# Kernel optimization log

Hardware: AMD Instinct MI355X
Metric: run time of the kernel (lower is better)

Reference implementation:

```python
import jax, jax.numpy as jnp
import numpy as np

NHEAD = 16
EPS = 1e-5

def layer_norm(x, g, b):
    mu = jnp.mean(x, axis=-1, keepdims=True)
    var = jnp.mean(jnp.square(x - mu), axis=-1, keepdims=True)
    return (x - mu) * jax.lax.rsqrt(var + EPS) * g + b

def setup_inputs() -> dict:
    key = jax.random.key(0)
    ks = jax.random.split(key, 12)
    d_model, d_hid = 1024, 4096  # MHA num_hiddens == dim_feedforward (source quirk)
    B, S = 2, 2048
    s_in = 1.0 / np.sqrt(d_model)
    s_hid = 1.0 / np.sqrt(d_hid)
    return {
        "x": jax.random.normal(ks[0], (B, S, d_model), jnp.float32),
        "Wq": jax.random.normal(ks[1], (d_model, d_hid), jnp.float32) * s_in,
        "Wk": jax.random.normal(ks[2], (d_model, d_hid), jnp.float32) * s_in,
        "Wv": jax.random.normal(ks[3], (d_model, d_hid), jnp.float32) * s_in,
        "Wo": jax.random.normal(ks[4], (d_hid, d_model), jnp.float32) * s_hid,
        "W1": jax.random.normal(ks[5], (d_model, d_hid), jnp.float32) * s_in,
        "b1": jnp.zeros((d_hid,), jnp.float32),
        "W2": jax.random.normal(ks[6], (d_hid, d_model), jnp.float32) * s_hid,
        "b2": jnp.zeros((d_model,), jnp.float32),
        "g1": jnp.ones((d_model,), jnp.float32),
        "be1": jnp.zeros((d_model,), jnp.float32),
        "g2": jnp.ones((d_model,), jnp.float32),
        "be2": jnp.zeros((d_model,), jnp.float32),
    }

def reference(x, Wq, Wk, Wv, Wo, W1, b1, W2, b2, g1, be1, g2, be2):
    B, S, D = x.shape
    H = NHEAD
    # pre-norm attention branch (dropout = identity at eval)
    x1 = layer_norm(x, g1, be1)
    q = (x1 @ Wq).reshape(B, S, H, -1)  # [B,S,H,dh], dh = num_hiddens/H
    k = (x1 @ Wk).reshape(B, S, H, -1)
    v = (x1 @ Wv).reshape(B, S, H, -1)
    dh = q.shape[-1]
    scores = jnp.einsum('bqhd,bkhd->bhqk', q, k) / jnp.sqrt(jnp.float32(dh))
    attn = jax.nn.softmax(scores, axis=-1)
    ctx = jnp.einsum('bhqk,bkhd->bqhd', attn, v).reshape(B, S, -1)
    x = x + ctx @ Wo
    # pre-norm FFN branch
    x2 = layer_norm(x, g2, be2)
    h = jax.nn.relu(x2 @ W1 + b1)
    out = x + (h @ W2 + b2)
    return out
```

## Files before the change

### kernel.cpp

```cpp
#include <hip/hip_runtime.h>
#include <hip/hip_bf16.h>
#include <stdint.h>

using bf16x8 = __attribute__((ext_vector_type(8))) __bf16;
using f32x4  = __attribute__((ext_vector_type(4))) float;

__device__ __forceinline__ uint16_t f2bf(float f) {
    uint32_t u = __builtin_bit_cast(uint32_t, f);
    u += 0x7FFFu + ((u >> 16) & 1u);
    return (uint16_t)(u >> 16);
}
__device__ __forceinline__ uint32_t pack2bf(float lo, float hi) {
    return (uint32_t)f2bf(lo) | ((uint32_t)f2bf(hi) << 16);
}

__device__ __forceinline__ void gld_lds16(const void* g, void* l) {
    __builtin_amdgcn_global_load_lds(
        (const __attribute__((address_space(1))) void*)g,
        (__attribute__((address_space(3))) void*)l,
        16, 0, 0);
}

__global__ __launch_bounds__(256)
void wconv(const float* __restrict__ in, uint16_t* __restrict__ out, int R, int C) {
    __shared__ float t[32][33];
    int c0 = blockIdx.x * 32, r0 = blockIdx.y * 32;
    int tx = threadIdx.x & 31, ty = threadIdx.x >> 5;
    #pragma unroll
    for (int i = 0; i < 32; i += 8)
        t[ty + i][tx] = in[(size_t)(r0 + ty + i) * C + c0 + tx];
    __syncthreads();
    #pragma unroll
    for (int i = 0; i < 32; i += 8)
        out[(size_t)(c0 + ty + i) * R + r0 + tx] = f2bf(t[tx][ty + i]);
}

__global__ __launch_bounds__(256)
void ln_bf16(const float* __restrict__ x, const float* __restrict__ gw,
             const float* __restrict__ bw, uint16_t* __restrict__ out) {
    const int D = 1024;
    int row = blockIdx.x;
    float4 v = ((const float4*)(x + (size_t)row * D))[threadIdx.x];
    float s  = v.x + v.y + v.z + v.w;
    float ss = v.x * v.x + v.y * v.y + v.z * v.z + v.w * v.w;
    #pragma unroll
    for (int m = 1; m < 64; m <<= 1) {
        s  += __shfl_xor(s, m);
        ss += __shfl_xor(ss, m);
    }
    __shared__ float red[8];
    int wid = threadIdx.x >> 6, lane = threadIdx.x & 63;
    if (lane == 0) { red[wid] = s; red[4 + wid] = ss; }
    __syncthreads();
    s  = red[0] + red[1] + red[2] + red[3];
    ss = red[4] + red[5] + red[6] + red[7];
    float mu  = s * (1.f / 1024.f);
    float var = ss * (1.f / 1024.f) - mu * mu;
    float rstd = rsqrtf(var + 1e-5f);
    float4 gv = ((const float4*)gw)[threadIdx.x];
    float4 bv = ((const float4*)bw)[threadIdx.x];
    ushort4 o;
    o.x = f2bf((v.x - mu) * rstd * gv.x + bv.x);
    o.y = f2bf((v.y - mu) * rstd * gv.y + bv.y);
    o.z = f2bf((v.z - mu) * rstd * gv.z + bv.z);
    o.w = f2bf((v.w - mu) * rstd * gv.w + bv.w);
    ((ushort4*)(out + (size_t)row * D))[threadIdx.x] = o;
}

template <int EPI>
__global__ __launch_bounds__(256, 2)
void gemm_bt(const uint16_t* __restrict__ A, const uint16_t* __restrict__ B,
             void* __restrict__ Cp, const float* __restrict__ bias,
             const float* __restrict__ resid, int M, int N, int K) {
    __shared__ uint16_t sA[128 * 32];
    __shared__ uint16_t sB[128 * 32];
    int bid = blockIdx.x;
    int cpx = gridDim.x >> 3;
    bid = (bid & 7) * cpx + (bid >> 3);
    int nbn  = N >> 7;
    int brow = (bid / nbn) << 7;
    int bcol = (bid % nbn) << 7;
    int t = threadIdx.x;
    int wid = t >> 6, lane = t & 63;
    int wr = (wid >> 1) << 6, wc = (wid & 1) << 6;
    int q = lane & 15, g = lane >> 4;

    f32x4 acc[4][4] = {};

    const uint16_t* Abase = A + (size_t)brow * K + ((lane & 3) << 3);
    const uint16_t* Bbase = B + (size_t)bcol * K + ((lane & 3) << 3);
    int rsub = lane >> 2;

    for (int kt = 0; kt < K; kt += 32) {
        __syncthreads();
        #pragma unroll
        for (int i = 0; i < 2; ++i) {
            int chunk = i * 4 + wid;
            int row = chunk * 16 + rsub;
            gld_lds16(Abase + (size_t)row * K + kt, &sA[chunk * 512]);
            gld_lds16(Bbase + (size_t)row * K + kt, &sB[chunk * 512]);
        }
        __syncthreads();
        bf16x8 af[4], bfr[4];
        #pragma unroll
        for (int i = 0; i < 4; ++i)
            af[i] = *(const bf16x8*)&sA[(wr + i * 16 + q) * 32 + g * 8];
        #pragma unroll
        for (int j = 0; j < 4; ++j)
            bfr[j] = *(const bf16x8*)&sB[(wc + j * 16 + q) * 32 + g * 8];
        #pragma unroll
        for (int i = 0; i < 4; ++i)
            #pragma unroll
            for (int j = 0; j < 4; ++j)
                acc[i][j] = __builtin_amdgcn_mfma_f32_16x16x32_bf16(
                    af[i], bfr[j], acc[i][j], 0, 0, 0);
    }

    float* Cf = (float*)Cp;
    #pragma unroll
    for (int i = 0; i < 4; ++i) {
        #pragma unroll
        for (int j = 0; j < 4; ++j) {
            #pragma unroll
            for (int r = 0; r < 4; ++r) {
                int gr = brow + wr + i * 16 + g * 4 + r;
                int gc = bcol + wc + j * 16 + q;
                float v = acc[i][j][r];
                size_t idx = (size_t)gr * N + gc;
                if constexpr (EPI == 2) {
                    Cf[idx] = v + bias[gc] + resid[idx];
                } else {
                    Cf[idx] = v + resid[idx];
                }
            }
        }
    }
}

template <int EPI>
__global__ __launch_bounds__(512, 2)
void gemm256(const uint16_t* __restrict__ A, const uint16_t* __restrict__ B,
             void* __restrict__ Cp, const float* __restrict__ bias,
             int M, int N, int K) {
    __shared__ uint8_t smem[131072];
    int bid = blockIdx.x;
    int cpx = gridDim.x >> 3;
    bid = (bid & 7) * cpx + (bid >> 3);
    int nbn  = N >> 8;
    int brow = (bid / nbn) << 8;
    int bcol = (bid % nbn) << 8;
    int t0 = threadIdx.x;
    int wid = t0 >> 6, lane = t0 & 63;
    int wr = wid >> 2, wc = wid & 3;
    int q = lane & 15, g = lane >> 4;

    const uint16_t* Asw = A + (size_t)(brow + (lane >> 3)) * K + (((lane & 7) ^ (lane >> 3)) << 3);
    const uint16_t* Bsw = B + (size_t)(bcol + (lane >> 3)) * K + (((lane & 7) ^ (lane >> 3)) << 3);

    f32x4 acc[2][2][4][2] = {};
    int NKT = K >> 6;

#define STAGE256(BSEL, KK)                                                     \
    {                                                                          \
        uint8_t* dA = smem + (BSEL) * 32768;                                   \
        uint8_t* dB = smem + 65536 + (BSEL) * 32768;                           \
        _Pragma("unroll")                                                      \
        for (int i = 0; i < 4; ++i) {                                          \
            int c = wid * 4 + i;                                               \
            gld_lds16(Asw + (size_t)(c * 8) * K + (KK), dA + c * 1024);        \
            gld_lds16(Bsw + (size_t)(c * 8) * K + (KK), dB + c * 1024);        \
        }                                                                      \
    }

    STAGE256(0, 0)

    for (int t = 0; t < NKT; ++t) {
        int cur = t & 1;
        if (t + 1 < NKT) {
            STAGE256(cur ^ 1, (t + 1) << 6)
            asm volatile("s_waitcnt vmcnt(8)" ::: "memory");
        } else {
            asm volatile("s_waitcnt vmcnt(0)" ::: "memory");
        }
        __builtin_amdgcn_sched_barrier(0);
        __builtin_amdgcn_s_barrier();
        __builtin_amdgcn_sched_barrier(0);

        const uint8_t* bA = smem + cur * 32768;
        const uint8_t* bB = smem + 65536 + cur * 32768;

        bf16x8 af[4][2], bfr[2][2];

#define LOADA256(MH)                                                           \
        _Pragma("unroll")                                                      \
        for (int m2 = 0; m2 < 4; ++m2)                                         \
            _Pragma("unroll")                                                  \
            for (int ks = 0; ks < 2; ++ks) {                                   \
                int rr = wr * 128 + (MH) * 64 + m2 * 16 + q;                   \
                int sl = (ks * 4 + g) ^ (q & 7);                               \
                af[m2][ks] = *(const bf16x8*)(bA + rr * 128 + sl * 16);        \
            }
#define LOADB256(NH)                                                           \
        _Pragma("unroll")                                                      \
        for (int n2 = 0; n2 < 2; ++n2)                                         \
            _Pragma("unroll")                                                  \
            for (int ks = 0; ks < 2; ++ks) {                                   \
                int cc = wc * 64 + (NH) * 32 + n2 * 16 + q;                    \
                int sl = (ks * 4 + g) ^ (q & 7);                               \
                bfr[n2][ks] = *(const bf16x8*)(bB + cc * 128 + sl * 16);       \
            }
#define MMQ256(MH, NH)                                                         \
        __builtin_amdgcn_s_setprio(1);                                         \
        _Pragma("unroll")                                                      \
        for (int m2 = 0; m2 < 4; ++m2)                                         \
            _Pragma("unroll")                                                  \
            for (int n2 = 0; n2 < 2; ++n2)                                     \
                _Pragma("unroll")                                              \
                for (int ks = 0; ks < 2; ++ks)                                 \
                    acc[MH][NH][m2][n2] = __builtin_amdgcn_mfma_f32_16x16x32_bf16( \
                        af[m2][ks], bfr[n2][ks], acc[MH][NH][m2][n2], 0, 0, 0);\
        __builtin_amdgcn_s_setprio(0);

        LOADA256(0) LOADB256(0) MMQ256(0, 0)
        LOADB256(1) MMQ256(0, 1)
        LOADA256(1) MMQ256(1, 1)
        LOADB256(0) MMQ256(1, 0)

        __builtin_amdgcn_s_barrier();
    }

    uint16_t* Cb = (uint16_t*)Cp;
    #pragma unroll
    for (int mh = 0; mh < 2; ++mh)
        #pragma unroll
        for (int nh = 0; nh < 2; ++nh)
            #pragma unroll
            for (int m2 = 0; m2 < 4; ++m2)
                #pragma unroll
                for (int n2 = 0; n2 < 2; ++n2)
                    #pragma unroll
                    for (int r = 0; r < 4; ++r) {
                        int gr = brow + wr * 128 + mh * 64 + m2 * 16 + g * 4 + r;
                        int gc = bcol + wc * 64 + nh * 32 + n2 * 16 + q;
                        float v = acc[mh][nh][m2][n2][r];
                        if constexpr (EPI == 1) {
                            v += bias[gc];
                            v = v > 0.f ? v : 0.f;
                        }
                        Cb[(size_t)gr * N + gc] = f2bf(v);
                    }
#undef STAGE256
#undef LOADA256
#undef LOADB256
#undef MMQ256
}

__device__ __forceinline__ void attn_stage(uint8_t* smem, int bufsel,
        const uint16_t* Kb0, const uint16_t* Vb0, int ktok, int wid, int lane) {
    #pragma unroll
    for (int i = 0; i < 4; ++i) {
        int chunk = wid * 4 + i;
        int r = 2 * chunk + (lane >> 5);
        int s = lane & 31;
        int cg = (s & ~7) | ((s ^ r) & 7);
        gld_lds16(Kb0 + (size_t)(ktok + r) * 8192 + cg * 8,
                  smem + bufsel * 16384 + chunk * 1024);
    }
    #pragma unroll
    for (int i = 0; i < 4; ++i) {
        int chunk = wid * 4 + i;
        int r = 16 * chunk + (lane >> 2);
        int s = lane & 3;
        int cg = s ^ (r & 3);
        gld_lds16(Vb0 + (size_t)r * 4096 + ktok + cg * 8,
                  smem + 32768 + bufsel * 16384 + chunk * 1024);
    }
}

__device__ __forceinline__ bf16x8 sm_pack(const f32x4* sacc, f32x4* acc,
                                          float& m_run, float& l_run,
                                          int q, int g) {
    float mx = fmaxf(fmaxf(fmaxf(sacc[0][0], sacc[0][1]), fmaxf(sacc[0][2], sacc[0][3])),
                     fmaxf(fmaxf(sacc[1][0], sacc[1][1]), fmaxf(sacc[1][2], sacc[1][3])));
    mx = fmaxf(mx, __shfl_xor(mx, 16));
    mx = fmaxf(mx, __shfl_xor(mx, 32));
    if (!__all(mx - m_run <= 8.f)) {
        float m_new = fmaxf(m_run, mx);
        float alpha = __expf(m_run - m_new);
        l_run *= alpha;
        #pragma unroll
        for (int td = 0; td < 16; ++td) {
            acc[td][0] *= alpha; acc[td][1] *= alpha;
            acc[td][2] *= alpha; acc[td][3] *= alpha;
        }
        m_run = m_new;
    }
    float p[8]; float rs = 0.f;
    #pragma unroll
    for (int tm = 0; tm < 2; ++tm)
        #pragma unroll
        for (int r = 0; r < 4; ++r) {
            float e = __expf(sacc[tm][r] - m_run);
            p[tm * 4 + r] = e; rs += e;
        }
    rs += __shfl_xor(rs, 16);
    rs += __shfl_xor(rs, 32);
    l_run += rs;

    uint32_t pk0 = pack2bf(p[0], p[1]);
    uint32_t pk1 = pack2bf(p[2], p[3]);
    uint32_t pk2 = pack2bf(p[4], p[5]);
    uint32_t pk3 = pack2bf(p[6], p[7]);
    int srcA = ((g & 1) << 5) + q;
    int srcB = srcA + 16;
    uint32_t a0 = __shfl(pk0, srcA), a1 = __shfl(pk2, srcA);
    uint32_t b0 = __shfl(pk1, srcA), b1 = __shfl(pk3, srcA);
    uint32_t c0 = __shfl(pk0, srcB), c1 = __shfl(pk2, srcB);
    uint32_t d0 = __shfl(pk1, srcB), d1 = __shfl(pk3, srcB);
    bool hi = g >= 2;
    uint4 pb;
    pb.x = hi ? a1 : a0;
    pb.y = hi ? b1 : b0;
    pb.z = hi ? c1 : c0;
    pb.w = hi ? d1 : d0;
    return __builtin_bit_cast(bf16x8, pb);
}

__global__ __launch_bounds__(256, 2)
void attn(const uint16_t* __restrict__ Qg, const uint16_t* __restrict__ Kg,
          const uint16_t* __restrict__ Vtg, uint16_t* __restrict__ Og) {
    const int S = 2048, NT = 64, QKS = 8192, OC = 4096;
    __shared__ uint8_t smem[65536];

    int id = blockIdx.x;
    id = (id & 7) * 64 + (id >> 3);
    int qb = id & 15, h = (id >> 4) & 15, b = id >> 8;

    int t = threadIdx.x;
    int wid = t >> 6, lane = t & 63;
    int q = lane & 15, g = lane >> 4;
    int tok0 = b * S + qb * 128 + wid * 32;

    bf16x8 qf0[8], qf1[8];
    {
        const uint16_t* qrow0 = Qg + (size_t)(tok0 + q) * QKS + h * 256 + g * 8;
        const uint16_t* qrow1 = Qg + (size_t)(tok0 + 16 + q) * QKS + h * 256 + g * 8;
        #pragma unroll
        for (int c = 0; c < 8; ++c) {
            bf16x8 r0 = *(const bf16x8*)(qrow0 + c * 32);
            bf16x8 r1 = *(const bf16x8*)(qrow1 + c * 32);
            #pragma unroll
            for (int i = 0; i < 8; ++i) {
                r0[i] = (__bf16)((float)r0[i] * 0.0625f);
                r1[i] = (__bf16)((float)r1[i] * 0.0625f);
            }
            qf0[c] = r0; qf1[c] = r1;
        }
    }

    f32x4 acc0[16] = {}, acc1[16] = {};
    float m0 = -1e30f, l0 = 0.f;
    float m1 = -1e30f, l1 = 0.f;

    const uint16_t* Kb0 = Kg + (size_t)(b * S) * QKS + h * 256;
    const uint16_t* Vb0 = Vtg + (size_t)(h * 256) * 4096 + b * S;

    attn_stage(smem, 0, Kb0, Vb0, 0, wid, lane);

    for (int kt = 0; kt < NT; ++kt) {
        int cb = (kt & 1) * 16384;
        if (kt + 1 < NT) {
            attn_stage(smem, (kt + 1) & 1, Kb0, Vb0, (kt + 1) * 32, wid, lane);
            asm volatile("s_waitcnt vmcnt(12)" ::: "memory");
        } else {
            asm volatile("s_waitcnt vmcnt(4)" ::: "memory");
        }
        __builtin_amdgcn_sched_barrier(0);
        __builtin_amdgcn_s_barrier();

        const uint16_t* sk = (const uint16_t*)(smem + cb);
        const uint16_t* sv = (const uint16_t*)(smem + 32768 + cb);

        f32x4 sA0[2] = {}, sA1[2] = {};
        __builtin_amdgcn_s_setprio(1);
        #pragma unroll
        for (int c = 0; c < 8; ++c) {
            #pragma unroll
            for (int tm = 0; tm < 2; ++tm) {
                int G = c * 4 + g;
                int slot = (G & ~7) | ((G ^ q) & 7);
                bf16x8 kf = *(const bf16x8*)(sk + (tm * 16 + q) * 256 + slot * 8);
                sA0[tm] = __builtin_amdgcn_mfma_f32_16x16x32_bf16(kf, qf0[c], sA0[tm], 0, 0, 0);
                sA1[tm] = __builtin_amdgcn_mfma_f32_16x16x32_bf16(kf, qf1[c], sA1[tm], 0, 0, 0);
            }
        }
        __builtin_amdgcn_s_setprio(0);

        bf16x8 pfrag0 = sm_pack(sA0, acc0, m0, l0, q, g);
        bf16x8 pfrag1 = sm_pack(sA1, acc1, m1, l1, q, g);

        if (kt + 1 < NT) {
            asm volatile("s_waitcnt vmcnt(8)" ::: "memory");
        } else {
            asm volatile("s_waitcnt vmcnt(0)" ::: "memory");
        }
        __builtin_amdgcn_sched_barrier(0);
        __builtin_amdgcn_s_barrier();

        int sl = g ^ (q & 3);
        __builtin_amdgcn_s_setprio(1);
        #pragma unroll
        for (int td = 0; td < 16; ++td) {
            bf16x8 vf = *(const bf16x8*)(sv + (td * 16 + q) * 32 + sl * 8);
            acc0[td] = __builtin_amdgcn_mfma_f32_16x16x32_bf16(vf, pfrag0, acc0[td], 0, 0, 0);
            acc1[td] = __builtin_amdgcn_mfma_f32_16x16x32_bf16(vf, pfrag1, acc1[td], 0, 0, 0);
        }
        __builtin_amdgcn_s_setprio(0);
        __builtin_amdgcn_s_barrier();
    }

    __syncthreads();
    {
        float inv0 = 1.f / l0, inv1 = 1.f / l1;
        uint32_t* w0 = (uint32_t*)(smem + wid * 16384);
        uint32_t* w1 = (uint32_t*)(smem + wid * 16384 + 8192);
        #pragma unroll
        for (int td = 0; td < 16; ++td) {
            int base = (q * 256 + td * 16 + g * 4) >> 1;
            w0[base]     = pack2bf(acc0[td][0] * inv0, acc0[td][1] * inv0);
            w0[base + 1] = pack2bf(acc0[td][2] * inv0, acc0[td][3] * inv0);
            w1[base]     = pack2bf(acc1[td][0] * inv1, acc1[td][1] * inv1);
            w1[base + 1] = pack2bf(acc1[td][2] * inv1, acc1[td][3] * inv1);
        }
    }
    __syncthreads();
    #pragma unroll
    for (int s2 = 0; s2 < 2; ++s2) {
        const uint16_t* tb = (const uint16_t*)(smem + wid * 16384 + s2 * 8192);
        #pragma unroll
        for (int r2 = 0; r2 < 8; ++r2) {
            int c = r2 * 64 + lane;
            int qq = c >> 5, dc = c & 31;
            uint4 v = *(const uint4*)&tb[qq * 256 + dc * 8];
            *(uint4*)(Og + (size_t)(tok0 + s2 * 16 + qq) * OC + h * 256 + dc * 8) = v;
        }
    }
}

extern "C" void kernel_launch(void* const* d_in, const int* in_sizes, int n_in,
                              void* d_out, int out_size, void* d_ws, size_t ws_size,
                              hipStream_t stream) {
    const float* x   = (const float*)d_in[0];
    const float* Wq  = (const float*)d_in[1];
    const float* Wk  = (const float*)d_in[2];
    const float* Wv  = (const float*)d_in[3];
    const float* Wo  = (const float*)d_in[4];
    const float* W1  = (const float*)d_in[5];
    const float* b1  = (const float*)d_in[6];
    const float* W2  = (const float*)d_in[7];
    const float* b2  = (const float*)d_in[8];
    const float* g1  = (const float*)d_in[9];
    const float* be1 = (const float*)d_in[10];
    const float* g2  = (const float*)d_in[11];
    const float* be2 = (const float*)d_in[12];

    char* ws = (char*)d_ws;
    const size_t M8 = 8388608;
    uint16_t* WqkT = (uint16_t*)(ws + 0 * M8);
    uint16_t* WqT  = WqkT;
    uint16_t* WkT  = (uint16_t*)(ws + 1 * M8);
    uint16_t* WvT  = (uint16_t*)(ws + 2 * M8);
    uint16_t* WoT  = (uint16_t*)(ws + 3 * M8);
    uint16_t* W1T  = (uint16_t*)(ws + 4 * M8);
    uint16_t* W2T  = (uint16_t*)(ws + 5 * M8);
    uint16_t* x1   = (uint16_t*)(ws + 6 * M8);
    uint16_t* x2   = (uint16_t*)(ws + 7 * M8);
    uint16_t* QK   = (uint16_t*)(ws + 8 * M8);
    uint16_t* Vt   = (uint16_t*)(ws + 16 * M8);
    uint16_t* ctx  = (uint16_t*)(ws + 20 * M8);
    float*    xmid = (float*)(ws + 12 * M8);
    uint16_t* Hn   = (uint16_t*)(ws + 8 * M8);

    wconv<<<dim3(128, 32), 256, 0, stream>>>(Wq, WqT, 1024, 4096);
    wconv<<<dim3(128, 32), 256, 0, stream>>>(Wk, WkT, 1024, 4096);
    wconv<<<dim3(128, 32), 256, 0, stream>>>(Wv, WvT, 1024, 4096);
    wconv<<<dim3(32, 128), 256, 0, stream>>>(Wo, WoT, 4096, 1024);
    wconv<<<dim3(128, 32), 256, 0, stream>>>(W1, W1T, 1024, 4096);
    wconv<<<dim3(32, 128), 256, 0, stream>>>(W2, W2T, 4096, 1024);

    ln_bf16<<<4096, 256, 0, stream>>>(x, g1, be1, x1);

    gemm256<0><<<512, 512, 0, stream>>>(x1, WqkT, QK, nullptr, 4096, 8192, 1024);
    gemm256<0><<<256, 512, 0, stream>>>(WvT, x1, Vt, nullptr, 4096, 4096, 1024);

    attn<<<512, 256, 0, stream>>>(QK, QK + 4096, Vt, ctx);

    gemm_bt<3><<<256, 256, 0, stream>>>(ctx, WoT, xmid, nullptr, x, 4096, 1024, 4096);

    ln_bf16<<<4096, 256, 0, stream>>>(xmid, g2, be2, x2);

    gemm256<1><<<256, 512, 0, stream>>>(x2, W1T, Hn, b1, 4096, 4096, 1024);
    gemm_bt<2><<<256, 256, 0, stream>>>(Hn, W2T, d_out, b2, xmid, 4096, 1024, 4096);
}
```

Measured before the change: 524.9 us.

## Pipeline 128-tile GEMM with double buffering, batch weight conversions, trim attention syncs

Replaces the simple 128x128 GEMM used for the Wo and W2 projections with a double-buffered version. It uses a BK=64 K-tile and an XOR-swizzled LDS layout, so global-to-LDS loads overlap MFMA work and a barrier is removed per iteration. The six weight-conversion launches are merged into three using blockIdx.z. In attention, the row-sum cross-lane shuffles move out of the inner loop to the end, and one barrier/waitcnt per tile is dropped by waiting for both K and V stages up front. The risks are larger LDS use, which may limit occupancy, and the V-stage wait now happening before the score compute.

```diff
diff --git a/kernel.cpp b/kernel.cpp
--- a/kernel.cpp
+++ b/kernel.cpp
@@ -22,7 +22,13 @@
 }
 
 __global__ __launch_bounds__(256)
-void wconv(const float* __restrict__ in, uint16_t* __restrict__ out, int R, int C) {
+void wconvB(const float* __restrict__ i0, const float* __restrict__ i1,
+            const float* __restrict__ i2, uint16_t* __restrict__ o0,
+            uint16_t* __restrict__ o1, uint16_t* __restrict__ o2,
+            int R, int C) {
+    int z = blockIdx.z;
+    const float* in = z == 0 ? i0 : (z == 1 ? i1 : i2);
+    uint16_t* out   = z == 0 ? o0 : (z == 1 ? o1 : o2);
     __shared__ float t[32][33];
     int c0 = blockIdx.x * 32, r0 = blockIdx.y * 32;
     int tx = threadIdx.x & 31, ty = threadIdx.x >> 5;
@@ -69,63 +75,95 @@
 
 template <int EPI>
 __global__ __launch_bounds__(256, 2)
-void gemm_bt(const uint16_t* __restrict__ A, const uint16_t* __restrict__ B,
-             void* __restrict__ Cp, const float* __restrict__ bias,
-             const float* __restrict__ resid, int M, int N, int K) {
-    __shared__ uint16_t sA[128 * 32];
-    __shared__ uint16_t sB[128 * 32];
+void gemm128p(const uint16_t* __restrict__ A, const uint16_t* __restrict__ B,
+              float* __restrict__ Cf, const float* __restrict__ bias,
+              const float* __restrict__ resid, int M, int N, int K) {
+    __shared__ uint8_t smem[65536];
     int bid = blockIdx.x;
     int cpx = gridDim.x >> 3;
     bid = (bid & 7) * cpx + (bid >> 3);
     int nbn  = N >> 7;
     int brow = (bid / nbn) << 7;
     int bcol = (bid % nbn) << 7;
-    int t = threadIdx.x;
-    int wid = t >> 6, lane = t & 63;
-    int wr = (wid >> 1) << 6, wc = (wid & 1) << 6;
+    int t0 = threadIdx.x;
+    int wid = t0 >> 6, lane = t0 & 63;
+    int wr = wid >> 1, wc = wid & 1;
     int q = lane & 15, g = lane >> 4;
 
+    const uint16_t* Asw = A + (size_t)(brow + (lane >> 3)) * K + (((lane & 7) ^ (lane >> 3)) << 3);
+    const uint16_t* Bsw = B + (size_t)(bcol + (lane >> 3)) * K + (((lane & 7) ^ (lane >> 3)) << 3);
+
     f32x4 acc[4][4] = {};
-
-    const uint16_t* Abase = A + (size_t)brow * K + ((lane & 3) << 3);
-    const uint16_t* Bbase = B + (size_t)bcol * K + ((lane & 3) << 3);
-    int rsub = lane >> 2;
-
-    for (int kt = 0; kt < K; kt += 32) {
-        __syncthreads();
-        #pragma unroll
-        for (int i = 0; i < 2; ++i) {
-            int chunk = i * 4 + wid;
-            int row = chunk * 16 + rsub;
-            gld_lds16(Abase + (size_t)row * K + kt, &sA[chunk * 512]);
-            gld_lds16(Bbase + (size_t)row * K + kt, &sB[chunk * 512]);
-        }
-        __syncthreads();
-        bf16x8 af[4], bfr[4];
-        #pragma unroll
-        for (int i = 0; i < 4; ++i)
-            af[i] = *(const bf16x8*)&sA[(wr + i * 16 + q) * 32 + g * 8];
-        #pragma unroll
-        for (int j = 0; j < 4; ++j)
-            bfr[j] = *(const bf16x8*)&sB[(wc + j * 16 + q) * 32 + g * 8];
-        #pragma unroll
-        for (int i = 0; i < 4; ++i)
-            #pragma unroll
-            for (int j = 0; j < 4; ++j)
-                acc[i][j] = __builtin_amdgcn_mfma_f32_16x16x32_bf16(
-                    af[i], bfr[j], acc[i][j], 0, 0, 0);
-    }
-
-    float* Cf = (float*)Cp;
-    #pragma unroll
-    for (int i = 0; i < 4; ++i) {
-        #pragma unroll
-        for (int j = 0; j < 4; ++j) {
+    int NKT = K >> 6;
+
+#define STG128(BSEL, KK)                                                       \
+    {                                                                          \
+        uint8_t* dA = smem + (BSEL) * 16384;                                   \
+        uint8_t* dB = smem + 32768 + (BSEL) * 16384;                           \
+        _Pragma("unroll")                                                      \
+        for (int i = 0; i < 4; ++i) {                                          \
+            int c = wid * 4 + i;                                               \
+            gld_lds16(Asw + (size_t)(c * 8) * K + (KK), dA + c * 1024);        \
+            gld_lds16(Bsw + (size_t)(c * 8) * K + (KK), dB + c * 1024);        \
+        }                                                                      \
+    }
+
+    STG128(0, 0)
+
+    for (int t = 0; t < NKT; ++t) {
+        int cur = t & 1;
+        if (t + 1 < NKT) {
+            STG128(cur ^ 1, (t + 1) << 6)
+            asm volatile("s_waitcnt vmcnt(8)" ::: "memory");
+        } else {
+            asm volatile("s_waitcnt vmcnt(0)" ::: "memory");
+        }
+        __builtin_amdgcn_sched_barrier(0);
+        __builtin_amdgcn_s_barrier();
+        __builtin_amdgcn_sched_barrier(0);
+
+        const uint8_t* bA = smem + cur * 16384;
+        const uint8_t* bB = smem + 32768 + cur * 16384;
+
+        bf16x8 af[4][2], bfr[4][2];
+        #pragma unroll
+        for (int m2 = 0; m2 < 4; ++m2)
+            #pragma unroll
+            for (int ks = 0; ks < 2; ++ks) {
+                int rr = wr * 64 + m2 * 16 + q;
+                int sl = (ks * 4 + g) ^ (q & 7);
+                af[m2][ks] = *(const bf16x8*)(bA + rr * 128 + sl * 16);
+            }
+        #pragma unroll
+        for (int n2 = 0; n2 < 4; ++n2)
+            #pragma unroll
+            for (int ks = 0; ks < 2; ++ks) {
+                int cc = wc * 64 + n2 * 16 + q;
+                int sl = (ks * 4 + g) ^ (q & 7);
+                bfr[n2][ks] = *(const bf16x8*)(bB + cc * 128 + sl * 16);
+            }
+        __builtin_amdgcn_s_setprio(1);
+        #pragma unroll
+        for (int m2 = 0; m2 < 4; ++m2)
+            #pragma unroll
+            for (int n2 = 0; n2 < 4; ++n2)
+                #pragma unroll
+                for (int ks = 0; ks < 2; ++ks)
+                    acc[m2][n2] = __builtin_amdgcn_mfma_f32_16x16x32_bf16(
+                        af[m2][ks], bfr[n2][ks], acc[m2][n2], 0, 0, 0);
+        __builtin_amdgcn_s_setprio(0);
+        __builtin_amdgcn_s_barrier();
+    }
+
+    #pragma unroll
+    for (int m2 = 0; m2 < 4; ++m2)
+        #pragma unroll
+        for (int n2 = 0; n2 < 4; ++n2)
             #pragma unroll
             for (int r = 0; r < 4; ++r) {
-                int gr = brow + wr + i * 16 + g * 4 + r;
-                int gc = bcol + wc + j * 16 + q;
-                float v = acc[i][j][r];
+                int gr = brow + wr * 64 + m2 * 16 + g * 4 + r;
+                int gc = bcol + wc * 64 + n2 * 16 + q;
+                float v = acc[m2][n2][r];
                 size_t idx = (size_t)gr * N + gc;
                 if constexpr (EPI == 2) {
                     Cf[idx] = v + bias[gc] + resid[idx];
@@ -133,8 +171,7 @@
                     Cf[idx] = v + resid[idx];
                 }
             }
-        }
-    }
+#undef STG128
 }
 
 template <int EPI>
@@ -303,8 +340,6 @@
             float e = __expf(sacc[tm][r] - m_run);
             p[tm * 4 + r] = e; rs += e;
         }
-    rs += __shfl_xor(rs, 16);
-    rs += __shfl_xor(rs, 32);
     l_run += rs;
 
     uint32_t pk0 = pack2bf(p[0], p[1]);
@@ -371,9 +406,9 @@
         int cb = (kt & 1) * 16384;
         if (kt + 1 < NT) {
             attn_stage(smem, (kt + 1) & 1, Kb0, Vb0, (kt + 1) * 32, wid, lane);
-            asm volatile("s_waitcnt vmcnt(12)" ::: "memory");
+            asm volatile("s_waitcnt vmcnt(8)" ::: "memory");
         } else {
-            asm volatile("s_waitcnt vmcnt(4)" ::: "memory");
+            asm volatile("s_waitcnt vmcnt(0)" ::: "memory");
         }
         __builtin_amdgcn_sched_barrier(0);
         __builtin_amdgcn_s_barrier();
@@ -399,14 +434,6 @@
         bf16x8 pfrag0 = sm_pack(sA0, acc0, m0, l0, q, g);
         bf16x8 pfrag1 = sm_pack(sA1, acc1, m1, l1, q, g);
 
-        if (kt + 1 < NT) {
-            asm volatile("s_waitcnt vmcnt(8)" ::: "memory");
-        } else {
-            asm volatile("s_waitcnt vmcnt(0)" ::: "memory");
-        }
-        __builtin_amdgcn_sched_barrier(0);
-        __builtin_amdgcn_s_barrier();
-
         int sl = g ^ (q & 3);
         __builtin_amdgcn_s_setprio(1);
         #pragma unroll
@@ -418,6 +445,9 @@
         __builtin_amdgcn_s_setprio(0);
         __builtin_amdgcn_s_barrier();
     }
+
+    l0 += __shfl_xor(l0, 16); l0 += __shfl_xor(l0, 32);
+    l1 += __shfl_xor(l1, 16); l1 += __shfl_xor(l1, 32);
 
     __syncthreads();
     {
@@ -481,12 +511,9 @@
     float*    xmid = (float*)(ws + 12 * M8);
     uint16_t* Hn   = (uint16_t*)(ws + 8 * M8);
 
-    wconv<<<dim3(128, 32), 256, 0, stream>>>(Wq, WqT, 1024, 4096);
-    wconv<<<dim3(128, 32), 256, 0, stream>>>(Wk, WkT, 1024, 4096);
-    wconv<<<dim3(128, 32), 256, 0, stream>>>(Wv, WvT, 1024, 4096);
-    wconv<<<dim3(32, 128), 256, 0, stream>>>(Wo, WoT, 4096, 1024);
-    wconv<<<dim3(128, 32), 256, 0, stream>>>(W1, W1T, 1024, 4096);
-    wconv<<<dim3(32, 128), 256, 0, stream>>>(W2, W2T, 4096, 1024);
+    wconvB<<<dim3(128, 32, 3), 256, 0, stream>>>(Wq, Wk, Wv, WqT, WkT, WvT, 1024, 4096);
+    wconvB<<<dim3(32, 128, 2), 256, 0, stream>>>(Wo, W2, nullptr, WoT, W2T, nullptr, 4096, 1024);
+    wconvB<<<dim3(128, 32, 1), 256, 0, stream>>>(W1, nullptr, nullptr, W1T, nullptr, nullptr, 1024, 4096);
 
     ln_bf16<<<4096, 256, 0, stream>>>(x, g1, be1, x1);
 
@@ -495,10 +522,10 @@
 
     attn<<<512, 256, 0, stream>>>(QK, QK + 4096, Vt, ctx);
 
-    gemm_bt<3><<<256, 256, 0, stream>>>(ctx, WoT, xmid, nullptr, x, 4096, 1024, 4096);
+    gemm128p<3><<<256, 256, 0, stream>>>(ctx, WoT, xmid, nullptr, x, 4096, 1024, 4096);
 
     ln_bf16<<<4096, 256, 0, stream>>>(xmid, g2, be2, x2);
 
     gemm256<1><<<256, 512, 0, stream>>>(x2, W1T, Hn, b1, 4096, 4096, 1024);
-    gemm_bt<2><<<256, 256, 0, stream>>>(Hn, W2T, d_out, b2, xmid, 4096, 1024, 4096);
-}
+    gemm128p<2><<<256, 256, 0, stream>>>(Hn, W2T, (float*)d_out, b2, xmid, 4096, 1024, 4096);
+}
```

Result: faster. 453.3 us, median of 2 (-13.7%).
